# Performance work log

Hardware: AMD Instinct MI355X
Metric: run time of the kernel (lower is better)

## Reference

```python
import jax, jax.numpy as jnp
import numpy as np

L, C, H, I, E, K = 2, 1024, 16, 4096, 8, 2
B, N = 4, 640
HD = C // H
SCALE = HD ** -0.5
EPS = 1e-6


def setup_inputs() -> dict:
    key = jax.random.key(0)
    ks = jax.random.split(key, 20)
    w = lambda k, shape: jax.random.normal(k, shape, dtype=jnp.float32) * 0.02
    return {
        "hidden_states": jax.random.normal(ks[0], (B, N, C), dtype=jnp.float32),
        "attention_mask": jnp.ones((B, N), dtype=jnp.int32),
        "relative_position_bias": jax.random.normal(ks[1], (H, N, N), dtype=jnp.float32),
        "qkv_w": w(ks[2], (L, 3 * C, C)),
        "q_bias": jnp.zeros((L, C), jnp.float32),
        "v_bias": jnp.zeros((L, C), jnp.float32),
        "proj_w": w(ks[3], (L, C, C)),
        "proj_b": jnp.zeros((L, C), jnp.float32),
        "ln1_s": jnp.ones((L, C), jnp.float32),
        "ln1_b": jnp.zeros((L, C), jnp.float32),
        "ln2_s": jnp.ones((L, C), jnp.float32),
        "ln2_b": jnp.zeros((L, C), jnp.float32),
        "gamma1": 0.1 * jnp.ones((L, C), jnp.float32),
        "gamma2": 0.1 * jnp.ones((L, C), jnp.float32),
        "gate_w": w(ks[4], (L, E, C)),
        "fc1_w": w(ks[5], (L, E, I, C)),
        "fc1_b": jnp.zeros((L, E, I), jnp.float32),
        "fc2_w": w(ks[6], (L, E, C, I)),
        "fc2_b": jnp.zeros((L, E, C), jnp.float32),
    }


def layer_norm(x, s, b):
    m = jnp.mean(x, axis=-1, keepdims=True)
    v = jnp.var(x, axis=-1, keepdims=True)
    return (x - m) * jax.lax.rsqrt(v + EPS) * s + b


def attention(x, mask, rpb, qkv_w, q_b, v_b, p_w, p_b):
    Bb, Nn, Cc = x.shape
    bias = jnp.concatenate([q_b, jnp.zeros_like(v_b), v_b])
    qkv = x @ qkv_w.T + bias  # [B,N,3C]
    qkv = qkv.reshape(Bb, Nn, 3, H, HD).transpose(2, 0, 3, 1, 4)  # [3,B,H,N,hd]
    q, k, v = qkv[0] * SCALE, qkv[1], qkv[2]
    attn = jnp.einsum("bhqd,bhkd->bhqk", q, k) + rpb[None]  # fp32 scores
    attn = jnp.where(mask[:, None, None, :].astype(bool), attn, -jnp.inf)
    attn = jax.nn.softmax(attn, axis=-1)
    out = jnp.einsum("bhqk,bhkd->bhqd", attn, v)
    out = out.transpose(0, 2, 1, 3).reshape(Bb, Nn, Cc)
    return out @ p_w.T + p_b


def moe_ffn(x, gate_w, fc1_w, fc1_b, fc2_w, fc2_b):
    # top-k softmax gating with renormalized combine weights (no capacity drop)
    logits = jnp.einsum("bnc,ec->bne", x, gate_w)
    probs = jax.nn.softmax(logits, axis=-1)  # [B,N,E]
    top_v, top_i = jax.lax.top_k(probs, K)  # [B,N,K]
    gates = top_v / jnp.sum(top_v, axis=-1, keepdims=True)
    onehot = jax.nn.one_hot(top_i, E, dtype=x.dtype)  # [B,N,K,E]
    combine = jnp.einsum("bnk,bnke->bne", gates, onehot)  # sparse combine weights
    # dense-per-expert compute (reference; mathematically == routed top-k)
    h = jnp.einsum("bnc,eic->bnei", x, fc1_w) + fc1_b
    h = jax.nn.gelu(h, approximate=False)
    y = jnp.einsum("bnei,eci->bnec", h, fc2_w) + fc2_b
    out = jnp.einsum("bnec,bne->bnc", y, combine)
    # load-balancing aux loss (Switch/GShard style)
    me = jnp.mean(probs.reshape(-1, E), axis=0)
    ce = jnp.mean(onehot.reshape(-1, E), axis=0) * K
    aux = E * jnp.sum(me * ce)
    return out, aux


def reference(hidden_states, attention_mask, relative_position_bias, qkv_w, q_bias,
              v_bias, proj_w, proj_b, ln1_s, ln1_b, ln2_s, ln2_b, gamma1, gamma2,
              gate_w, fc1_w, fc1_b, fc2_w, fc2_b):
    x = hidden_states
    aux_total = jnp.float32(0.0)
    for l in range(L):
        res = x
        h = layer_norm(x, ln1_s[l], ln1_b[l])
        h = attention(h, attention_mask, relative_position_bias,
                      qkv_w[l], q_bias[l], v_bias[l], proj_w[l], proj_b[l])
        x = res + h * gamma1[l]
        res = x
        h = layer_norm(x, ln2_s[l], ln2_b[l])
        h, aux = moe_ffn(h, gate_w[l], fc1_w[l], fc1_b[l], fc2_w[l], fc2_b[l])
        aux_total = aux_total + aux
        x = res + h * gamma2[l]
    return x, aux_total
```

## Files before the change

### kernel.cpp

```cpp
#include <hip/hip_runtime.h>
#include <hip/hip_bf16.h>

#define TB 4
#define TN 640
#define TC 1024
#define TH 16
#define THD 64
#define TI 4096
#define TE 8
#define TT (TB*TN)
#define TBH (TB*TH)
#define SCALE_ 0.125f
#define NT1 32
#define NT2 48

typedef unsigned short u16;
typedef __bf16 bf16x8 __attribute__((ext_vector_type(8)));
typedef float f32x4 __attribute__((ext_vector_type(4)));

__device__ __forceinline__ float gelu_tanh(float v){
  float t = 0.7978845608f*(v + 0.044715f*v*v*v);
  float e = __expf(2.f*t);
  return 0.5f*v*(1.f + (1.f - 2.f/(e + 1.f)));
}

template<int BM,int BN,int MODE,int EPI>
__global__ __launch_bounds__(512) void gemm8(
    const u16* __restrict__ A, const u16* __restrict__ Wb, void* __restrict__ Cout,
    const float* __restrict__ bias, long biasStride,
    const int* __restrict__ tE, const int* __restrict__ tL,
    const int* __restrict__ tC, const int* __restrict__ tO,
    const int* __restrict__ etok,
    int M, int Kfull, int Kchunk, int n0, int ldc, long sW, long sCk)
{
  constexpr int FM = BM/32, FN = BN/64;
  constexpr int AI = BM/64, BI = BN/64;

  const int nwg = gridDim.x;
  int lin = blockIdx.x;
  int q = nwg >> 3, r = nwg & 7;
  int xcd = lin & 7, pos = lin >> 3;
  int swz = (xcd < r ? xcd*(q+1) : r*(q+1) + (xcd-r)*q) + pos;
  const int id0 = swz % n0, id1 = swz / n0;

  int e, loc0, cnt, off0, bx;
  if constexpr (MODE == 0){
    e = 0; loc0 = id0*BM; cnt = M; off0 = 0; bx = id1;
  } else {
    bx = id0;
    e = tE[id1]; if (e < 0) return;
    loc0 = tL[id1]; cnt = tC[id1]; off0 = tO[id1];
  }
  const int kc = blockIdx.z;
  const long kbase = (long)kc * Kchunk;

  const int tid = threadIdx.x, w = tid>>6, lane = tid&63;
  const int wm = w>>2, wn = w&3;

  __shared__ __align__(16) u16 As0[BM*64], As1[BM*64];
  __shared__ __align__(16) u16 Bs0[BN*64], Bs1[BN*64];

  const u16* Wz = Wb + (long)e*sW;

  const int c16 = (lane&7) ^ ((lane>>3)&7);
  long a_src[AI];
  #pragma unroll
  for (int j=0;j<AI;j++){
    int li = (w*AI+j)*8 + (lane>>3);
    int row;
    if constexpr (MODE == 0){
      row = loc0 + li;
    } else {
      int ll = loc0 + li; if (ll > cnt-1) ll = cnt-1;
      if constexpr (MODE == 1) row = etok[e*TT + ll];
      else                     row = off0 + ll;
    }
    a_src[j] = (long)row*Kfull + kbase + c16*8;
  }
  long b_src[BI];
  #pragma unroll
  for (int j=0;j<BI;j++){
    int rr = bx*BN + (w*BI+j)*8 + (lane>>3);
    b_src[j] = (long)rr*Kfull + kbase + c16*8;
  }

  auto STAGE = [&](u16 (&Ad)[BM*64], u16 (&Bd)[BN*64], int t){
    #pragma unroll
    for (int j=0;j<AI;j++)
      __builtin_amdgcn_global_load_lds(
        (const __attribute__((address_space(1))) void*)(A + a_src[j] + t*64),
        (__attribute__((address_space(3))) void*)(&Ad[(w*AI+j)*512]), 16, 0, 0);
    #pragma unroll
    for (int j=0;j<BI;j++)
      __builtin_amdgcn_global_load_lds(
        (const __attribute__((address_space(1))) void*)(Wz + b_src[j] + t*64),
        (__attribute__((address_space(3))) void*)(&Bd[(w*BI+j)*512]), 16, 0, 0);
  };

  f32x4 acc[FM][FN];
  #pragma unroll
  for (int m=0;m<FM;m++)
    #pragma unroll
    for (int n=0;n<FN;n++) acc[m][n] = (f32x4){0.f,0.f,0.f,0.f};

  const int lr = lane & 15;
  const int s0 = (lane>>4) ^ (lane&7);
  const int abase = lr*128 + s0*16;

  auto COMP = [&](const u16 (&As)[BM*64], const u16 (&Bs)[BN*64]){
    const char* Ab = (const char*)&As[0];
    const char* Bb = (const char*)&Bs[0];
    bf16x8 af[FM][2], bfr[FN][2];
    #pragma unroll
    for (int m=0;m<FM;m++){
      af[m][0] = *reinterpret_cast<const bf16x8*>(Ab + wm*(BM/2)*128 + m*2048 + abase);
      af[m][1] = *reinterpret_cast<const bf16x8*>(Ab + wm*(BM/2)*128 + m*2048 + (abase^64));
    }
    #pragma unroll
    for (int n=0;n<FN;n++){
      bfr[n][0] = *reinterpret_cast<const bf16x8*>(Bb + wn*(BN/4)*128 + n*2048 + abase);
      bfr[n][1] = *reinterpret_cast<const bf16x8*>(Bb + wn*(BN/4)*128 + n*2048 + (abase^64));
    }
    #pragma unroll
    for (int m=0;m<FM;m++)
      #pragma unroll
      for (int n=0;n<FN;n++){
        acc[m][n] = __builtin_amdgcn_mfma_f32_16x16x32_bf16(af[m][0], bfr[n][0], acc[m][n], 0,0,0);
        acc[m][n] = __builtin_amdgcn_mfma_f32_16x16x32_bf16(af[m][1], bfr[n][1], acc[m][n], 0,0,0);
      }
  };

  const int nt = Kchunk >> 6;
  STAGE(As0, Bs0, 0);
  __syncthreads();
  for (int t=0; t<nt; t+=2){
    if (t+1 < nt) STAGE(As1, Bs1, t+1);
    COMP(As0, Bs0);
    __syncthreads();
    if (t+1 < nt){
      if (t+2 < nt) STAGE(As0, Bs0, t+2);
      COMP(As1, Bs1);
      __syncthreads();
    }
  }

  const float* bz = (bias && kc==0) ? (bias + (long)e*biasStride) : nullptr;
  #pragma unroll
  for (int m=0;m<FM;m++){
    #pragma unroll
    for (int n=0;n<FN;n++){
      int gcol = bx*BN + wn*(BN/4) + n*16 + (lane&15);
      float bv = bz ? bz[gcol] : 0.f;
      #pragma unroll
      for (int jj=0;jj<4;jj++){
        int li = wm*(BM/2) + m*16 + (lane>>4)*4 + jj;
        int ll = loc0 + li;
        if (MODE != 0 && ll >= cnt) continue;
        float v = acc[m][n][jj] + bv;
        if constexpr (EPI == 3) v = gelu_tanh(v);
        long orow = (MODE == 0) ? (long)ll : (long)(off0 + ll);
        ((__hip_bfloat16*)Cout)[kc*sCk + orow*ldc + gcol] = __float2bfloat16(v);
      }
    }
  }
}

template<int BM,int BN,int EPI>
__global__ __launch_bounds__(256) void gemm_bt(
    const u16* __restrict__ A, const u16* __restrict__ Wb, void* __restrict__ Cout,
    const float* __restrict__ bias, const float* __restrict__ scalevec,
    int M, int Kfull, int nby, int ldc)
{
  constexpr int FM = BM/32, FN = BN/32;
  constexpr int AI = BM/32, BI = BN/32;

  const int nwg = gridDim.x;
  int lin = blockIdx.x;
  int q = nwg >> 3, r = nwg & 7;
  int xcd = lin & 7, pos = lin >> 3;
  int swz = (xcd < r ? xcd*(q+1) : r*(q+1) + (xcd-r)*q) + pos;
  const int bx = swz / nby;
  const int by = swz - bx*nby;
  if (by*BM >= M) return;

  const int tid = threadIdx.x, w = tid>>6, lane = tid&63;
  const int wm = w>>1, wn = w&1;

  __shared__ __align__(16) u16 As0[BM*64], As1[BM*64];
  __shared__ __align__(16) u16 Bs0[BN*64], Bs1[BN*64];

  const int c16 = (lane&7) ^ ((lane>>3)&7);
  long a_src[AI];
  #pragma unroll
  for (int j=0;j<AI;j++){
    int i = by*BM + (w*AI+j)*8 + (lane>>3);
    a_src[j] = (long)i*Kfull + c16*8;
  }
  long b_src[BI];
  #pragma unroll
  for (int j=0;j<BI;j++){
    int rr = bx*BN + (w*BI+j)*8 + (lane>>3);
    b_src[j] = (long)rr*Kfull + c16*8;
  }

  auto STAGE = [&](u16 (&Ad)[BM*64], u16 (&Bd)[BN*64], int t){
    #pragma unroll
    for (int j=0;j<AI;j++)
      __builtin_amdgcn_global_load_lds(
        (const __attribute__((address_space(1))) void*)(A + a_src[j] + t*64),
        (__attribute__((address_space(3))) void*)(&Ad[(w*AI+j)*512]), 16, 0, 0);
    #pragma unroll
    for (int j=0;j<BI;j++)
      __builtin_amdgcn_global_load_lds(
        (const __attribute__((address_space(1))) void*)(Wb + b_src[j] + t*64),
        (__attribute__((address_space(3))) void*)(&Bd[(w*BI+j)*512]), 16, 0, 0);
  };

  f32x4 acc[FM][FN];
  #pragma unroll
  for (int m=0;m<FM;m++)
    #pragma unroll
    for (int n=0;n<FN;n++) acc[m][n] = (f32x4){0.f,0.f,0.f,0.f};

  const int lr = lane & 15;
  const int s0 = (lane>>4) ^ (lane&7);
  const int abase = lr*128 + s0*16;

  auto COMP = [&](const u16 (&As)[BM*64], const u16 (&Bs)[BN*64]){
    const char* Ab = (const char*)&As[0];
    const char* Bb = (const char*)&Bs[0];
    bf16x8 af[FM][2], bfr[FN][2];
    #pragma unroll
    for (int m=0;m<FM;m++){
      af[m][0] = *reinterpret_cast<const bf16x8*>(Ab + wm*(BM/2)*128 + m*2048 + abase);
      af[m][1] = *reinterpret_cast<const bf16x8*>(Ab + wm*(BM/2)*128 + m*2048 + (abase^64));
    }
    #pragma unroll
    for (int n=0;n<FN;n++){
      bfr[n][0] = *reinterpret_cast<const bf16x8*>(Bb + wn*(BN/2)*128 + n*2048 + abase);
      bfr[n][1] = *reinterpret_cast<const bf16x8*>(Bb + wn*(BN/2)*128 + n*2048 + (abase^64));
    }
    #pragma unroll
    for (int m=0;m<FM;m++)
      #pragma unroll
      for (int n=0;n<FN;n++){
        acc[m][n] = __builtin_amdgcn_mfma_f32_16x16x32_bf16(af[m][0], bfr[n][0], acc[m][n], 0,0,0);
        acc[m][n] = __builtin_amdgcn_mfma_f32_16x16x32_bf16(af[m][1], bfr[n][1], acc[m][n], 0,0,0);
      }
  };

  const int nt = Kfull >> 6;
  STAGE(As0, Bs0, 0);
  __syncthreads();
  for (int t=0; t<nt; t+=2){
    if (t+1 < nt) STAGE(As1, Bs1, t+1);
    COMP(As0, Bs0);
    __syncthreads();
    if (t+1 < nt){
      if (t+2 < nt) STAGE(As0, Bs0, t+2);
      COMP(As1, Bs1);
      __syncthreads();
    }
  }

  #pragma unroll
  for (int m=0;m<FM;m++){
    #pragma unroll
    for (int n=0;n<FN;n++){
      int gcol = bx*BN + wn*(BN/2) + n*16 + (lane&15);
      float bv = bias ? bias[gcol] : 0.f;
      #pragma unroll
      for (int jj=0;jj<4;jj++){
        int i = by*BM + wm*(BM/2) + m*16 + (lane>>4)*4 + jj;
        float v = acc[m][n][jj] + bv;
        float* p = (float*)Cout + (long)i*ldc + gcol;
        *p += v * scalevec[gcol];
      }
    }
  }
}

__global__ __launch_bounds__(256) void fattn(
    const u16* __restrict__ qkv, const u16* __restrict__ vT,
    const float* __restrict__ rpb, const int* __restrict__ mask, u16* __restrict__ attn_o)
{
  const int blk = blockIdx.x;
  const int bh = blk / 5, qt = blk - bh*5;
  const int b = bh >> 4, h = bh & 15;
  const int q0 = qt * 128;
  const int tid = threadIdx.x, w = tid >> 6, lane = tid & 63;

  __shared__ __align__(16) u16 Qs[128*64];
  __shared__ __align__(16) u16 Ks0[64*64], Ks1[64*64];
  __shared__ __align__(16) u16 Vs0[64*64], Vs1[64*64];
  __shared__ __align__(16) u16 Ps[4][32*72];

  const int c16 = (lane&7) ^ ((lane>>3)&7);
  const long qkbase = (long)h*THD;
  #pragma unroll
  for (int j=0;j<4;j++){
    int row = (w*4+j)*8 + (lane>>3);
    __builtin_amdgcn_global_load_lds(
      (const __attribute__((address_space(1))) void*)(qkv + (long)(b*TN + q0 + row)*(3*TC) + qkbase + c16*8),
      (__attribute__((address_space(3))) void*)(&Qs[(w*4+j)*512]), 16, 0, 0);
  }

  auto STAGE = [&](u16 (&Kd)[64*64], u16 (&Vd)[64*64], int k0){
    #pragma unroll
    for (int j=0;j<2;j++){
      int row = (w*2+j)*8 + (lane>>3);
      __builtin_amdgcn_global_load_lds(
        (const __attribute__((address_space(1))) void*)(qkv + (long)(b*TN + k0 + row)*(3*TC) + TC + qkbase + c16*8),
        (__attribute__((address_space(3))) void*)(&Kd[(w*2+j)*512]), 16, 0, 0);
      __builtin_amdgcn_global_load_lds(
        (const __attribute__((address_space(1))) void*)(vT + ((long)bh*THD + row)*TN + k0 + c16*8),
        (__attribute__((address_space(3))) void*)(&Vd[(w*2+j)*512]), 16, 0, 0);
    }
  };

  const int s0 = (lane>>4) ^ (lane&7);
  const int lr = lane & 15;

  f32x4 acc_o[2][4];
  #pragma unroll
  for (int mq=0;mq<2;mq++)
    #pragma unroll
    for (int nd=0;nd<4;nd++) acc_o[mq][nd] = (f32x4){0.f,0.f,0.f,0.f};
  float m_r[2][4], l_r[2][4];
  #pragma unroll
  for (int mq=0;mq<2;mq++)
    #pragma unroll
    for (int jj=0;jj<4;jj++){ m_r[mq][jj] = -3e38f; l_r[mq][jj] = 0.f; }

  auto TILE = [&](const u16 (&Ks)[64*64], const u16 (&Vs)[64*64], int k0){
    const char* Qb = (const char*)&Qs[0];
    const char* Kb = (const char*)&Ks[0];
    const char* Vb = (const char*)&Vs[0];
    bf16x8 qa[2][2], kf[4][2];
    #pragma unroll
    for (int mq=0;mq<2;mq++){
      int row = w*32 + mq*16 + lr;
      qa[mq][0] = *reinterpret_cast<const bf16x8*>(Qb + row*128 + s0*16);
      qa[mq][1] = *reinterpret_cast<const bf16x8*>(Qb + row*128 + (s0*16^64));
    }
    #pragma unroll
    for (int nk=0;nk<4;nk++){
      int row = nk*16 + lr;
      kf[nk][0] = *reinterpret_cast<const bf16x8*>(Kb + row*128 + s0*16);
      kf[nk][1] = *reinterpret_cast<const bf16x8*>(Kb + row*128 + (s0*16^64));
    }
    f32x4 acc_s[2][4];
    #pragma unroll
    for (int mq=0;mq<2;mq++)
      #pragma unroll
      for (int nk=0;nk<4;nk++){
        acc_s[mq][nk] = (f32x4){0.f,0.f,0.f,0.f};
        acc_s[mq][nk] = __builtin_amdgcn_mfma_f32_16x16x32_bf16(qa[mq][0], kf[nk][0], acc_s[mq][nk], 0,0,0);
        acc_s[mq][nk] = __builtin_amdgcn_mfma_f32_16x16x32_bf16(qa[mq][1], kf[nk][1], acc_s[mq][nk], 0,0,0);
      }
    float sc[2][4];
    #pragma unroll
    for (int mq=0;mq<2;mq++){
      #pragma unroll
      for (int jj=0;jj<4;jj++){
        int qrow = q0 + w*32 + mq*16 + (lane>>4)*4 + jj;
        float s[4];
        #pragma unroll
        for (int nk=0;nk<4;nk++){
          int kg = k0 + nk*16 + lr;
          float t = acc_s[mq][nk][jj]*SCALE_ + rpb[((long)h*TN + qrow)*TN + kg];
          if (mask[b*TN + kg] == 0) t = -1e30f;
          s[nk] = t;
        }
        float mx = fmaxf(fmaxf(s[0],s[1]), fmaxf(s[2],s[3]));
        #pragma unroll
        for (int o=1;o<16;o<<=1) mx = fmaxf(mx, __shfl_xor(mx, o));
        float mnew = fmaxf(m_r[mq][jj], mx);
        float scale = __expf(m_r[mq][jj] - mnew);
        float rs = 0.f;
        #pragma unroll
        for (int nk=0;nk<4;nk++){ s[nk] = __expf(s[nk] - mnew); rs += s[nk]; }
        #pragma unroll
        for (int o=1;o<16;o<<=1) rs += __shfl_xor(rs, o);
        l_r[mq][jj] = l_r[mq][jj]*scale + rs;
        m_r[mq][jj] = mnew;
        sc[mq][jj] = scale;
        int qloc = mq*16 + (lane>>4)*4 + jj;
        #pragma unroll
        for (int nk=0;nk<4;nk++)
          Ps[w][qloc*72 + nk*16 + lr] = (u16)__bfloat16_as_ushort(__float2bfloat16(s[nk]));
      }
      f32x4 sv = (f32x4){sc[mq][0], sc[mq][1], sc[mq][2], sc[mq][3]};
      #pragma unroll
      for (int nd=0;nd<4;nd++) acc_o[mq][nd] *= sv;
    }
    const char* Pw = (const char*)&Ps[w][0];
    bf16x8 pa[2][2], vb[4][2];
    #pragma unroll
    for (int mq=0;mq<2;mq++){
      int qloc = mq*16 + lr;
      pa[mq][0] = *reinterpret_cast<const bf16x8*>(Pw + qloc*144 + (lane>>4)*16);
      pa[mq][1] = *reinterpret_cast<const bf16x8*>(Pw + qloc*144 + (lane>>4)*16 + 64);
    }
    #pragma unroll
    for (int nd=0;nd<4;nd++){
      int row = nd*16 + lr;
      vb[nd][0] = *reinterpret_cast<const bf16x8*>(Vb + row*128 + s0*16);
      vb[nd][1] = *reinterpret_cast<const bf16x8*>(Vb + row*128 + (s0*16^64));
    }
    #pragma unroll
    for (int mq=0;mq<2;mq++)
      #pragma unroll
      for (int nd=0;nd<4;nd++){
        acc_o[mq][nd] = __builtin_amdgcn_mfma_f32_16x16x32_bf16(pa[mq][0], vb[nd][0], acc_o[mq][nd], 0,0,0);
        acc_o[mq][nd] = __builtin_amdgcn_mfma_f32_16x16x32_bf16(pa[mq][1], vb[nd][1], acc_o[mq][nd], 0,0,0);
      }
  };

  STAGE(Ks0, Vs0, 0);
  __syncthreads();
  for (int t=0; t<10; t+=2){
    if (t+1 < 10) STAGE(Ks1, Vs1, (t+1)*64);
    TILE(Ks0, Vs0, t*64);
    __syncthreads();
    if (t+1 < 10){
      if (t+2 < 10) STAGE(Ks0, Vs0, (t+2)*64);
      TILE(Ks1, Vs1, (t+1)*64);
      __syncthreads();
    }
  }

  #pragma unroll
  for (int mq=0;mq<2;mq++){
    float linv[4];
    #pragma unroll
    for (int jj=0;jj<4;jj++) linv[jj] = 1.f / l_r[mq][jj];
    #pragma unroll
    for (int nd=0;nd<4;nd++){
      #pragma unroll
      for (int jj=0;jj<4;jj++){
        int qg = q0 + w*32 + mq*16 + (lane>>4)*4 + jj;
        int dg = h*THD + nd*16 + lr;
        attn_o[(long)(b*TN + qg)*TC + dg] =
          (u16)__bfloat16_as_ushort(__float2bfloat16(acc_o[mq][nd][jj]*linv[jj]));
      }
    }
  }
}

__global__ __launch_bounds__(256) void v_transpose(const u16* __restrict__ qkv,
    u16* __restrict__ vT)
{
  const int bh = blockIdx.y, b = bh>>4, h = bh&15;
  const int n0 = blockIdx.x*128;
  const int tid = threadIdx.x;
  __shared__ u16 vt[128][72];
  #pragma unroll
  for (int j=0;j<4;j++){
    int f = j*2048 + tid*8;
    int r = f>>6, d = f&63;
    *(uint4*)(&vt[r][d]) = *(const uint4*)(qkv + (long)(b*TN + n0 + r)*(3*TC) + 2*TC + h*THD + d);
  }
  __syncthreads();
  #pragma unroll
  for (int j=0;j<4;j++){
    int f = j*2048 + tid*8;
    int dr = f>>7, nc = f&127;
    union { uint4 v; u16 u[8]; } o;
    #pragma unroll
    for (int e=0;e<8;e++) o.u[e] = vt[nc+e][dr];
    *(uint4*)(vT + ((long)bh*THD + dr)*TN + n0 + nc) = o.v;
  }
}

__global__ __launch_bounds__(256) void cvt2(
    const float* __restrict__ s1, u16* __restrict__ d1, long n1,
    const float* __restrict__ s2, u16* __restrict__ d2, long n2)
{
  long i = ((long)blockIdx.x*256 + threadIdx.x)*8;
  const float* s; u16* d; long k;
  if (i < n1){ s = s1; d = d1; k = i; }
  else { k = i - n1; if (k >= n2) return; s = s2; d = d2; }
  float4 a = *(const float4*)(s+k);
  float4 b = *(const float4*)(s+k+4);
  union { __hip_bfloat162 h[4]; uint4 v; } o;
  o.h[0] = __float22bfloat162_rn(make_float2(a.x,a.y));
  o.h[1] = __float22bfloat162_rn(make_float2(a.z,a.w));
  o.h[2] = __float22bfloat162_rn(make_float2(b.x,b.y));
  o.h[3] = __float22bfloat162_rn(make_float2(b.z,b.w));
  *(uint4*)(d+k) = o.v;
}

__global__ __launch_bounds__(256) void init_x_kernel(const float* __restrict__ h,
    float* __restrict__ x, int n)
{
  int i = blockIdx.x*256 + threadIdx.x;
  if (i < n) x[i] = h[i];
  else if (i == n) x[i] = 0.f;
}

__global__ __launch_bounds__(256) void ln_kernel(const float* __restrict__ x,
    const float* __restrict__ s, const float* __restrict__ b,
    float* __restrict__ of, __hip_bfloat16* __restrict__ ob)
{
  int row = blockIdx.x, tid = threadIdx.x;
  const float* xr = x + (long)row*TC;
  int c = tid*4;
  float4 xv = *(const float4*)(xr + c);
  float sum = xv.x+xv.y+xv.z+xv.w;
  float sq = xv.x*xv.x+xv.y*xv.y+xv.z*xv.z+xv.w*xv.w;
  #pragma unroll
  for (int o=32;o;o>>=1){ sum += __shfl_down(sum,o); sq += __shfl_down(sq,o); }
  __shared__ float ls[8];
  if ((tid&63)==0){ ls[tid>>6] = sum; ls[4+(tid>>6)] = sq; }
  __syncthreads();
  float mean = (ls[0]+ls[1]+ls[2]+ls[3]) * (1.f/TC);
  float ex2  = (ls[4]+ls[5]+ls[6]+ls[7]) * (1.f/TC);
  float rstd = rsqrtf(ex2 - mean*mean + 1e-6f);
  float4 sv = *(const float4*)(s + c);
  float4 bv = *(const float4*)(b + c);
  float o0 = (xv.x-mean)*rstd*sv.x + bv.x;
  float o1 = (xv.y-mean)*rstd*sv.y + bv.y;
  float o2 = (xv.z-mean)*rstd*sv.z + bv.z;
  float o3 = (xv.w-mean)*rstd*sv.w + bv.w;
  if (of) *(float4*)(of + (long)row*TC + c) = make_float4(o0,o1,o2,o3);
  __hip_bfloat16* op = ob + (long)row*TC + c;
  *reinterpret_cast<__hip_bfloat162*>(op)   = __float22bfloat162_rn(make_float2(o0,o1));
  *reinterpret_cast<__hip_bfloat162*>(op+2) = __float22bfloat162_rn(make_float2(o2,o3));
}

__global__ void build_qkv_bias(const float* __restrict__ qb, const float* __restrict__ vb,
    float* __restrict__ out)
{
  int i = blockIdx.x*256 + threadIdx.x;
  if (i >= 3*TC) return;
  float v = 0.f;
  if (i < TC) v = qb[i];
  else if (i >= 2*TC) v = vb[i-2*TC];
  out[i] = v;
}

__global__ __launch_bounds__(256) void gate_kernel(const float* __restrict__ ln,
    const float* __restrict__ gw, float* __restrict__ logits,
    int* __restrict__ counts, float* __restrict__ psum)
{
  int t = blockIdx.x, tid = threadIdx.x;
  if (t == 0 && tid < TE){ counts[tid] = 0; psum[tid] = 0.f; }
  int c = tid*4;
  float4 xv = *(const float4*)(ln + (long)t*TC + c);
  __shared__ float ls[4];
  for (int e=0;e<TE;e++){
    float4 wv = *(const float4*)(gw + (long)e*TC + c);
    float p = xv.x*wv.x + xv.y*wv.y + xv.z*wv.z + xv.w*wv.w;
    #pragma unroll
    for (int o=32;o;o>>=1) p += __shfl_down(p,o);
    if ((tid&63)==0) ls[tid>>6] = p;
    __syncthreads();
    if (tid==0) logits[(long)t*TE + e] = ls[0]+ls[1]+ls[2]+ls[3];
    __syncthreads();
  }
}

__global__ __launch_bounds__(256) void routing_kernel(const float* __restrict__ logits,
    int* __restrict__ counts, int* __restrict__ etok,
    int* __restrict__ tEt, int* __restrict__ tPt, float* __restrict__ tGt,
    float* __restrict__ psum)
{
  __shared__ float ps[TE];
  int tid = threadIdx.x;
  if (tid < TE) ps[tid] = 0.f;
  __syncthreads();
  int t = blockIdx.x*256 + tid;
  if (t < TT){
    float pr[TE]; float mx = -3e38f;
    #pragma unroll
    for (int e=0;e<TE;e++){ pr[e] = logits[(long)t*TE+e]; mx = fmaxf(mx, pr[e]); }
    float sum = 0.f;
    #pragma unroll
    for (int e=0;e<TE;e++){ pr[e] = __expf(pr[e]-mx); sum += pr[e]; }
    float inv = 1.f/sum;
    #pragma unroll
    for (int e=0;e<TE;e++) pr[e] *= inv;
    int i1 = 0;
    #pragma unroll
    for (int e=1;e<TE;e++) if (pr[e] > pr[i1]) i1 = e;
    int i2 = -1;
    #pragma unroll
    for (int e=0;e<TE;e++){ if (e==i1) continue; if (i2<0 || pr[e]>pr[i2]) i2=e; }
    float p1 = pr[i1], p2 = pr[i2];
    float g1 = p1/(p1+p2), g2 = p2/(p1+p2);
    int pos1 = atomicAdd(&counts[i1], 1);
    etok[i1*TT + pos1] = t;
    int pos2 = atomicAdd(&counts[i2], 1);
    etok[i2*TT + pos2] = t;
    tEt[2*t] = i1; tPt[2*t] = pos1; tGt[2*t] = g1;
    tEt[2*t+1] = i2; tPt[2*t+1] = pos2; tGt[2*t+1] = g2;
    #pragma unroll
    for (int e=0;e<TE;e++) atomicAdd(&ps[e], pr[e]);
  }
  __syncthreads();
  if (tid < TE) atomicAdd(&psum[tid], ps[tid]);
}

__global__ void finalize_routing(const int* __restrict__ counts, int* __restrict__ offsets,
    const float* __restrict__ psum, float* __restrict__ aux,
    int* __restrict__ tE1, int* __restrict__ tL1, int* __restrict__ tC1, int* __restrict__ tO1,
    int* __restrict__ tE2, int* __restrict__ tL2, int* __restrict__ tC2, int* __restrict__ tO2)
{
  int off = 0; float a = 0.f; int n1 = 0, n2 = 0;
  for (int e=0;e<TE;e++){
    offsets[e] = off; int c = counts[e];
    for (int j=0;j<c;j+=256){ tE1[n1]=e; tL1[n1]=j; tC1[n1]=c; tO1[n1]=off; n1++; }
    for (int j=0;j<c;j+=128){ tE2[n2]=e; tL2[n2]=j; tC2[n2]=c; tO2[n2]=off; n2++; }
    a += (psum[e]*(1.f/TT)) * ((float)c*(1.f/TT));
    off += c;
  }
  for (;n1<NT1;n1++) tE1[n1] = -1;
  for (;n2<NT2;n2++) tE2[n2] = -1;
  aux[0] += (float)TE * a;
}

__global__ __launch_bounds__(256) void combine_kernel(
    const u16* __restrict__ y, long yck, const int* __restrict__ tEt,
    const int* __restrict__ tPt, const float* __restrict__ tGt,
    const int* __restrict__ offsets, const float* __restrict__ gamma2,
    float* __restrict__ x)
{
  int t = blockIdx.x, c = threadIdx.x*4;
  int e1 = tEt[2*t], e2 = tEt[2*t+1];
  long s1 = (long)(offsets[e1]+tPt[2*t])*TC + c;
  long s2 = (long)(offsets[e2]+tPt[2*t+1])*TC + c;
  float g1 = tGt[2*t], g2 = tGt[2*t+1];
  ushort4 a0 = *(const ushort4*)(y+s1);
  ushort4 a1 = *(const ushort4*)(y+yck+s1);
  ushort4 b0 = *(const ushort4*)(y+s2);
  ushort4 b1 = *(const ushort4*)(y+yck+s2);
  float4 gv = *(const float4*)(gamma2 + c);
  float* xp = x + (long)t*TC + c;
  float4 xv = *(const float4*)xp;
  auto f = [](u16 u){ union{float f;unsigned i;} v; v.i = (unsigned)u<<16; return v.f; };
  xv.x += (g1*(f(a0.x)+f(a1.x)) + g2*(f(b0.x)+f(b1.x)))*gv.x;
  xv.y += (g1*(f(a0.y)+f(a1.y)) + g2*(f(b0.y)+f(b1.y)))*gv.y;
  xv.z += (g1*(f(a0.z)+f(a1.z)) + g2*(f(b0.z)+f(b1.z)))*gv.z;
  xv.w += (g1*(f(a0.w)+f(a1.w)) + g2*(f(b0.w)+f(b1.w)))*gv.w;
  *(float4*)xp = xv;
}

extern "C" void kernel_launch(void* const* d_in, const int* in_sizes, int n_in,
                              void* d_out, int out_size, void* d_ws, size_t ws_size,
                              hipStream_t stream) {
  (void)in_sizes; (void)n_in; (void)out_size; (void)ws_size;
  const float* hidden = (const float*)d_in[0];
  const int*   amask  = (const int*)d_in[1];
  const float* rpb    = (const float*)d_in[2];
  const float* qkv_w  = (const float*)d_in[3];
  const float* q_bias = (const float*)d_in[4];
  const float* v_bias = (const float*)d_in[5];
  const float* proj_w = (const float*)d_in[6];
  const float* proj_b = (const float*)d_in[7];
  const float* ln1_s  = (const float*)d_in[8];
  const float* ln1_b  = (const float*)d_in[9];
  const float* ln2_s  = (const float*)d_in[10];
  const float* ln2_b  = (const float*)d_in[11];
  const float* gamma1 = (const float*)d_in[12];
  const float* gamma2 = (const float*)d_in[13];
  const float* gate_w = (const float*)d_in[14];
  const float* fc1_w  = (const float*)d_in[15];
  const float* fc1_b  = (const float*)d_in[16];
  const float* fc2_w  = (const float*)d_in[17];
  const float* fc2_b  = (const float*)d_in[18];

  float* x = (float*)d_out;
  const int NXC = TT*TC;

  char* p = (char*)d_ws;
  auto alloc = [&](size_t bytes)->void* {
    void* r = (void*)p; p += (bytes + 255) & ~(size_t)255; return r;
  };
  float* qkvbias = (float*)alloc(3*TC*4);
  u16*   ln_bf   = (u16*)alloc((size_t)TT*TC*2);
  float* ln_f    = (float*)alloc((size_t)TT*TC*4);
  float* logits  = (float*)alloc((size_t)TT*TE*4);
  int*   counts  = (int*)alloc(TE*4);
  int*   offsets = (int*)alloc(TE*4);
  float* psum    = (float*)alloc(TE*4);
  int*   etok    = (int*)alloc((size_t)TE*TT*4);
  int*   tEt     = (int*)alloc((size_t)2*TT*4);
  int*   tPt     = (int*)alloc((size_t)2*TT*4);
  float* tGt     = (float*)alloc((size_t)2*TT*4);
  int*   tE1 = (int*)alloc(NT1*4); int* tL1 = (int*)alloc(NT1*4);
  int*   tC1 = (int*)alloc(NT1*4); int* tO1 = (int*)alloc(NT1*4);
  int*   tE2 = (int*)alloc(NT2*4); int* tL2 = (int*)alloc(NT2*4);
  int*   tC2 = (int*)alloc(NT2*4); int* tO2 = (int*)alloc(NT2*4);
  char* arena = (char*)alloc(202375168);
  u16*   qkv_bf  = (u16*)(arena + 157286400);
  u16*   vT      = (u16*)(arena + 183500800);
  u16*   attn_o  = (u16*)(arena + 188743680);
  u16*   wqkv    = (u16*)(arena + 193986560);
  u16*   wproj   = (u16*)(arena + 200278016);
  u16*   fc1b    = (u16*)(arena);
  u16*   fc2b    = (u16*)(arena + 67108864);
  u16*   h1      = (u16*)(arena + 134217728);
  u16*   yslot   = (u16*)(arena + 176160768);
  const long YCK = (long)5120*TC;

  init_x_kernel<<<(NXC+1+255)/256, 256, 0, stream>>>(hidden, x, NXC);

  for (int l=0;l<2;l++){
    ln_kernel<<<TT, 256, 0, stream>>>(x, ln1_s + l*TC, ln1_b + l*TC, nullptr, (__hip_bfloat16*)ln_bf);
    build_qkv_bias<<<(3*TC+255)/256, 256, 0, stream>>>(q_bias + l*TC, v_bias + l*TC, qkvbias);
    cvt2<<<(4*TC*TC)/2048, 256, 0, stream>>>(
        qkv_w + (size_t)l*3*TC*TC, wqkv, (long)3*TC*TC,
        proj_w + (size_t)l*TC*TC, wproj, (long)TC*TC);
    gemm8<256,128,0,1><<<dim3(240,1,1), 512, 0, stream>>>(
        ln_bf, wqkv, qkv_bf, qkvbias, 0,
        nullptr, nullptr, nullptr, nullptr, nullptr,
        TT, TC, TC, 10, 3*TC, 0, 0);
    v_transpose<<<dim3(TN/128, TBH), 256, 0, stream>>>(qkv_bf, vT);
    fattn<<<dim3(TBH*5,1,1), 256, 0, stream>>>(qkv_bf, vT, rpb, amask, attn_o);
    cvt2<<<(2*TE*TI*TC)/2048, 256, 0, stream>>>(
        fc1_w + (size_t)l*TE*TI*TC, fc1b, (long)TE*TI*TC,
        fc2_w + (size_t)l*TE*TC*TI, fc2b, (long)TE*TC*TI);
    gemm_bt<64,128,2><<<dim3(8*40,1,1), 256, 0, stream>>>(
        attn_o, wproj, x, proj_b + l*TC, gamma1 + l*TC,
        TT, TC, 40, TC);

    ln_kernel<<<TT, 256, 0, stream>>>(x, ln2_s + l*TC, ln2_b + l*TC, ln_f, (__hip_bfloat16*)ln_bf);
    gate_kernel<<<TT, 256, 0, stream>>>(ln_f, gate_w + (size_t)l*TE*TC, logits, counts, psum);
    routing_kernel<<<(TT+255)/256, 256, 0, stream>>>(logits, counts, etok, tEt, tPt, tGt, psum);
    finalize_routing<<<1, 1, 0, stream>>>(counts, offsets, psum, x + NXC,
        tE1, tL1, tC1, tO1, tE2, tL2, tC2, tO2);
    gemm8<256,256,1,3><<<dim3(16*NT1,1,1), 512, 0, stream>>>(
        ln_bf, fc1b, h1, fc1_b + (size_t)l*TE*TI, TI,
        tE1, tL1, tC1, tO1, etok,
        0, TC, TC, 16, TI, (long)TI*TC, 0);
    gemm8<128,256,2,1><<<dim3(4*NT2,1,2), 512, 0, stream>>>(
        h1, fc2b, yslot, fc2_b + (size_t)l*TE*TC, TC,
        tE2, tL2, tC2, tO2, nullptr,
        0, TI, TI/2, 4, TC, (long)TC*TI, YCK);
    combine_kernel<<<TT, 256, 0, stream>>>(yslot, YCK, tEt, tPt, tGt, offsets, gamma2 + l*TC, x);
  }
}
```

Baseline: 980.0 us.

## Fuse LayerNorm into gate and combine kernels, retile QKV and FC2 GEMMs

Merges the second LayerNorm with the gating projection so the fp32 LN output buffer is no longer written and reread. The next layer's first LayerNorm is folded into the MoE combine kernel, which removes one standalone LN launch and one read of x per layer. The QKV and FC2 GEMM tiles are halved in one dimension to launch more blocks, trading per-block reuse for better occupancy across CUs. The gate now uses fp32 LN values held in registers, matching the old fp32 path.

```diff
diff --git a/kernel.cpp b/kernel.cpp
--- a/kernel.cpp
+++ b/kernel.cpp
@@ -501,7 +501,7 @@
 
 __global__ __launch_bounds__(256) void ln_kernel(const float* __restrict__ x,
     const float* __restrict__ s, const float* __restrict__ b,
-    float* __restrict__ of, __hip_bfloat16* __restrict__ ob)
+    __hip_bfloat16* __restrict__ ob)
 {
   int row = blockIdx.x, tid = threadIdx.x;
   const float* xr = x + (long)row*TC;
@@ -523,40 +523,50 @@
   float o1 = (xv.y-mean)*rstd*sv.y + bv.y;
   float o2 = (xv.z-mean)*rstd*sv.z + bv.z;
   float o3 = (xv.w-mean)*rstd*sv.w + bv.w;
-  if (of) *(float4*)(of + (long)row*TC + c) = make_float4(o0,o1,o2,o3);
   __hip_bfloat16* op = ob + (long)row*TC + c;
   *reinterpret_cast<__hip_bfloat162*>(op)   = __float22bfloat162_rn(make_float2(o0,o1));
   *reinterpret_cast<__hip_bfloat162*>(op+2) = __float22bfloat162_rn(make_float2(o2,o3));
 }
 
-__global__ void build_qkv_bias(const float* __restrict__ qb, const float* __restrict__ vb,
-    float* __restrict__ out)
-{
-  int i = blockIdx.x*256 + threadIdx.x;
-  if (i >= 3*TC) return;
-  float v = 0.f;
-  if (i < TC) v = qb[i];
-  else if (i >= 2*TC) v = vb[i-2*TC];
-  out[i] = v;
-}
-
-__global__ __launch_bounds__(256) void gate_kernel(const float* __restrict__ ln,
-    const float* __restrict__ gw, float* __restrict__ logits,
-    int* __restrict__ counts, float* __restrict__ psum)
-{
-  int t = blockIdx.x, tid = threadIdx.x;
-  if (t == 0 && tid < TE){ counts[tid] = 0; psum[tid] = 0.f; }
+__global__ __launch_bounds__(256) void ln_gate_kernel(const float* __restrict__ x,
+    const float* __restrict__ s, const float* __restrict__ b,
+    __hip_bfloat16* __restrict__ ob, const float* __restrict__ gw,
+    float* __restrict__ logits, int* __restrict__ counts, float* __restrict__ psum)
+{
+  int row = blockIdx.x, tid = threadIdx.x;
+  if (row == 0 && tid < TE){ counts[tid] = 0; psum[tid] = 0.f; }
+  const float* xr = x + (long)row*TC;
   int c = tid*4;
-  float4 xv = *(const float4*)(ln + (long)t*TC + c);
-  __shared__ float ls[4];
+  float4 xv = *(const float4*)(xr + c);
+  float sum = xv.x+xv.y+xv.z+xv.w;
+  float sq = xv.x*xv.x+xv.y*xv.y+xv.z*xv.z+xv.w*xv.w;
+  #pragma unroll
+  for (int o=32;o;o>>=1){ sum += __shfl_down(sum,o); sq += __shfl_down(sq,o); }
+  __shared__ float ls[8];
+  if ((tid&63)==0){ ls[tid>>6] = sum; ls[4+(tid>>6)] = sq; }
+  __syncthreads();
+  float mean = (ls[0]+ls[1]+ls[2]+ls[3]) * (1.f/TC);
+  float ex2  = (ls[4]+ls[5]+ls[6]+ls[7]) * (1.f/TC);
+  float rstd = rsqrtf(ex2 - mean*mean + 1e-6f);
+  float4 sv = *(const float4*)(s + c);
+  float4 bv = *(const float4*)(b + c);
+  float o0 = (xv.x-mean)*rstd*sv.x + bv.x;
+  float o1 = (xv.y-mean)*rstd*sv.y + bv.y;
+  float o2 = (xv.z-mean)*rstd*sv.z + bv.z;
+  float o3 = (xv.w-mean)*rstd*sv.w + bv.w;
+  __hip_bfloat16* op = ob + (long)row*TC + c;
+  *reinterpret_cast<__hip_bfloat162*>(op)   = __float22bfloat162_rn(make_float2(o0,o1));
+  *reinterpret_cast<__hip_bfloat162*>(op+2) = __float22bfloat162_rn(make_float2(o2,o3));
+  __shared__ float gs[4];
+  #pragma unroll
   for (int e=0;e<TE;e++){
     float4 wv = *(const float4*)(gw + (long)e*TC + c);
-    float p = xv.x*wv.x + xv.y*wv.y + xv.z*wv.z + xv.w*wv.w;
-    #pragma unroll
-    for (int o=32;o;o>>=1) p += __shfl_down(p,o);
-    if ((tid&63)==0) ls[tid>>6] = p;
+    float pr = o0*wv.x + o1*wv.y + o2*wv.z + o3*wv.w;
+    #pragma unroll
+    for (int o=32;o;o>>=1) pr += __shfl_down(pr,o);
+    if ((tid&63)==0) gs[tid>>6] = pr;
     __syncthreads();
-    if (tid==0) logits[(long)t*TE + e] = ls[0]+ls[1]+ls[2]+ls[3];
+    if (tid==0) logits[(long)row*TE + e] = gs[0]+gs[1]+gs[2]+gs[3];
     __syncthreads();
   }
 }
@@ -602,6 +612,17 @@
   if (tid < TE) atomicAdd(&psum[tid], ps[tid]);
 }
 
+__global__ void build_qkv_bias(const float* __restrict__ qb, const float* __restrict__ vb,
+    float* __restrict__ out)
+{
+  int i = blockIdx.x*256 + threadIdx.x;
+  if (i >= 3*TC) return;
+  float v = 0.f;
+  if (i < TC) v = qb[i];
+  else if (i >= 2*TC) v = vb[i-2*TC];
+  out[i] = v;
+}
+
 __global__ void finalize_routing(const int* __restrict__ counts, int* __restrict__ offsets,
     const float* __restrict__ psum, float* __restrict__ aux,
     int* __restrict__ tE1, int* __restrict__ tL1, int* __restrict__ tC1, int* __restrict__ tO1,
@@ -620,13 +641,15 @@
   aux[0] += (float)TE * a;
 }
 
-__global__ __launch_bounds__(256) void combine_kernel(
+__global__ __launch_bounds__(256) void combine_ln(
     const u16* __restrict__ y, long yck, const int* __restrict__ tEt,
     const int* __restrict__ tPt, const float* __restrict__ tGt,
     const int* __restrict__ offsets, const float* __restrict__ gamma2,
-    float* __restrict__ x)
-{
-  int t = blockIdx.x, c = threadIdx.x*4;
+    float* __restrict__ x,
+    const float* __restrict__ ln_s, const float* __restrict__ ln_b,
+    __hip_bfloat16* __restrict__ ln_out)
+{
+  int t = blockIdx.x, tid = threadIdx.x, c = tid*4;
   int e1 = tEt[2*t], e2 = tEt[2*t+1];
   long s1 = (long)(offsets[e1]+tPt[2*t])*TC + c;
   long s2 = (long)(offsets[e2]+tPt[2*t+1])*TC + c;
@@ -644,6 +667,26 @@
   xv.z += (g1*(f(a0.z)+f(a1.z)) + g2*(f(b0.z)+f(b1.z)))*gv.z;
   xv.w += (g1*(f(a0.w)+f(a1.w)) + g2*(f(b0.w)+f(b1.w)))*gv.w;
   *(float4*)xp = xv;
+  if (!ln_out) return;
+  float sum = xv.x+xv.y+xv.z+xv.w;
+  float sq = xv.x*xv.x+xv.y*xv.y+xv.z*xv.z+xv.w*xv.w;
+  #pragma unroll
+  for (int o=32;o;o>>=1){ sum += __shfl_down(sum,o); sq += __shfl_down(sq,o); }
+  __shared__ float ls[8];
+  if ((tid&63)==0){ ls[tid>>6] = sum; ls[4+(tid>>6)] = sq; }
+  __syncthreads();
+  float mean = (ls[0]+ls[1]+ls[2]+ls[3]) * (1.f/TC);
+  float ex2  = (ls[4]+ls[5]+ls[6]+ls[7]) * (1.f/TC);
+  float rstd = rsqrtf(ex2 - mean*mean + 1e-6f);
+  float4 sv = *(const float4*)(ln_s + c);
+  float4 bv = *(const float4*)(ln_b + c);
+  float o0 = (xv.x-mean)*rstd*sv.x + bv.x;
+  float o1 = (xv.y-mean)*rstd*sv.y + bv.y;
+  float o2 = (xv.z-mean)*rstd*sv.z + bv.z;
+  float o3 = (xv.w-mean)*rstd*sv.w + bv.w;
+  __hip_bfloat16* op = ln_out + (long)t*TC + c;
+  *reinterpret_cast<__hip_bfloat162*>(op)   = __float22bfloat162_rn(make_float2(o0,o1));
+  *reinterpret_cast<__hip_bfloat162*>(op+2) = __float22bfloat162_rn(make_float2(o2,o3));
 }
 
 extern "C" void kernel_launch(void* const* d_in, const int* in_sizes, int n_in,
@@ -679,7 +722,6 @@
   };
   float* qkvbias = (float*)alloc(3*TC*4);
   u16*   ln_bf   = (u16*)alloc((size_t)TT*TC*2);
-  float* ln_f    = (float*)alloc((size_t)TT*TC*4);
   float* logits  = (float*)alloc((size_t)TT*TE*4);
   int*   counts  = (int*)alloc(TE*4);
   int*   offsets = (int*)alloc(TE*4);
@@ -707,15 +749,16 @@
   init_x_kernel<<<(NXC+1+255)/256, 256, 0, stream>>>(hidden, x, NXC);
 
   for (int l=0;l<2;l++){
-    ln_kernel<<<TT, 256, 0, stream>>>(x, ln1_s + l*TC, ln1_b + l*TC, nullptr, (__hip_bfloat16*)ln_bf);
+    if (l == 0)
+      ln_kernel<<<TT, 256, 0, stream>>>(x, ln1_s, ln1_b, (__hip_bfloat16*)ln_bf);
     build_qkv_bias<<<(3*TC+255)/256, 256, 0, stream>>>(q_bias + l*TC, v_bias + l*TC, qkvbias);
     cvt2<<<(4*TC*TC)/2048, 256, 0, stream>>>(
         qkv_w + (size_t)l*3*TC*TC, wqkv, (long)3*TC*TC,
         proj_w + (size_t)l*TC*TC, wproj, (long)TC*TC);
-    gemm8<256,128,0,1><<<dim3(240,1,1), 512, 0, stream>>>(
+    gemm8<128,128,0,1><<<dim3(20*24,1,1), 512, 0, stream>>>(
         ln_bf, wqkv, qkv_bf, qkvbias, 0,
         nullptr, nullptr, nullptr, nullptr, nullptr,
-        TT, TC, TC, 10, 3*TC, 0, 0);
+        TT, TC, TC, 20, 3*TC, 0, 0);
     v_transpose<<<dim3(TN/128, TBH), 256, 0, stream>>>(qkv_bf, vT);
     fattn<<<dim3(TBH*5,1,1), 256, 0, stream>>>(qkv_bf, vT, rpb, amask, attn_o);
     cvt2<<<(2*TE*TI*TC)/2048, 256, 0, stream>>>(
@@ -725,8 +768,8 @@
         attn_o, wproj, x, proj_b + l*TC, gamma1 + l*TC,
         TT, TC, 40, TC);
 
-    ln_kernel<<<TT, 256, 0, stream>>>(x, ln2_s + l*TC, ln2_b + l*TC, ln_f, (__hip_bfloat16*)ln_bf);
-    gate_kernel<<<TT, 256, 0, stream>>>(ln_f, gate_w + (size_t)l*TE*TC, logits, counts, psum);
+    ln_gate_kernel<<<TT, 256, 0, stream>>>(x, ln2_s + l*TC, ln2_b + l*TC,
+        (__hip_bfloat16*)ln_bf, gate_w + (size_t)l*TE*TC, logits, counts, psum);
     routing_kernel<<<(TT+255)/256, 256, 0, stream>>>(logits, counts, etok, tEt, tPt, tGt, psum);
     finalize_routing<<<1, 1, 0, stream>>>(counts, offsets, psum, x + NXC,
         tE1, tL1, tC1, tO1, tE2, tL2, tC2, tO2);
@@ -734,10 +777,13 @@
         ln_bf, fc1b, h1, fc1_b + (size_t)l*TE*TI, TI,
         tE1, tL1, tC1, tO1, etok,
         0, TC, TC, 16, TI, (long)TI*TC, 0);
-    gemm8<128,256,2,1><<<dim3(4*NT2,1,2), 512, 0, stream>>>(
+    gemm8<128,128,2,1><<<dim3(8*NT2,1,2), 512, 0, stream>>>(
         h1, fc2b, yslot, fc2_b + (size_t)l*TE*TC, TC,
         tE2, tL2, tC2, tO2, nullptr,
-        0, TI, TI/2, 4, TC, (long)TC*TI, YCK);
-    combine_kernel<<<TT, 256, 0, stream>>>(yslot, YCK, tEt, tPt, tGt, offsets, gamma2 + l*TC, x);
-  }
-}
+        0, TI, TI/2, 8, TC, (long)TC*TI, YCK);
+    combine_ln<<<TT, 256, 0, stream>>>(yslot, YCK, tEt, tPt, tGt, offsets,
+        gamma2 + l*TC, x,
+        ln1_s + (l+1)*TC, ln1_b + (l+1)*TC,
+        (l == 0) ? (__hip_bfloat16*)ln_bf : nullptr);
+  }
+}
```

Result: faster. 906.9 us (-7.5%).
